# Performance work log

Hardware: AMD Instinct MI355X
Metric: run time of the kernel (lower is better)

The kernel has to match this reference:

```python
import jax, jax.numpy as jnp
import numpy as np

B, T, C, H = 4, 2048, 1024, 16
HD = C // H  # head_dim = 64


def setup_inputs() -> dict:
    key = jax.random.key(0)
    k1, k2, k3, k4, k5 = jax.random.split(key, 5)
    s = 1.0 / np.sqrt(C)
    return {
        "x": jax.random.normal(k1, (B, T, C), dtype=jnp.float32),
        "Wqkv": jax.random.normal(k2, (C, 3 * C), dtype=jnp.float32) * s,
        "bqkv": jnp.zeros((3 * C,), dtype=jnp.float32),
        "Wproj": jax.random.normal(k3, (C, C), dtype=jnp.float32) * s,
        "bproj": jnp.zeros((C,), dtype=jnp.float32),
    }


def reference(x, Wqkv, bqkv, Wproj, bproj):
    b, t, c = x.shape
    qkv = x @ Wqkv + bqkv                      # [B,T,3C]
    q, k, v = jnp.split(qkv, 3, axis=-1)
    # [B,T,C] -> [B,H,T,HD]
    q = q.reshape(b, t, H, HD).transpose(0, 2, 1, 3)
    k = k.reshape(b, t, H, HD).transpose(0, 2, 1, 3)
    v = v.reshape(b, t, H, HD).transpose(0, 2, 1, 3)
    att = jnp.einsum("bhqd,bhkd->bhqk", q, k) * (1.0 / np.sqrt(HD))
    causal = jnp.tril(jnp.ones((t, t), dtype=bool))
    att = jnp.where(causal[None, None], att, -jnp.inf)
    att = jax.nn.softmax(att, axis=-1)
    # dropout p=0.0 (eval) -> identity
    y = jnp.einsum("bhqk,bhkd->bhqd", att, v)  # [B,H,T,HD]
    y = y.transpose(0, 2, 1, 3).reshape(b, t, c)
    return y @ Wproj + bproj
```

## Files before the change

### kernel.cpp

```cpp
#include <hip/hip_runtime.h>


typedef unsigned short u16;
typedef short short8_t __attribute__((ext_vector_type(8)));
typedef float f32x4 __attribute__((ext_vector_type(4)));
typedef float f32x16 __attribute__((ext_vector_type(16)));
typedef unsigned int u32x4 __attribute__((ext_vector_type(4)));

#define B_ 4
#define T_ 2048
#define C_ 1024
#define H_ 16
#define HD_ 64
#define QSCALE 0.18033688011112042f

__device__ __forceinline__ u16 f32_to_bf16(float f) {
  unsigned int u = __float_as_uint(f);
  u += 0x7fffu + ((u >> 16) & 1u);
  return (u16)(u >> 16);
}

__device__ __forceinline__ void async_copy16(const void* g, void* l) {
  __builtin_amdgcn_global_load_lds((const __attribute__((address_space(1))) void*)g,
                                   (__attribute__((address_space(3))) void*)l, 16, 0, 0);
}

__device__ __forceinline__ void wave_barrier() { asm volatile("s_barrier" ::: "memory"); }
template <int N>
__device__ __forceinline__ void wait_vmcnt() {
  asm volatile("s_waitcnt vmcnt(%0)" ::"i"(N) : "memory");
}

__device__ __forceinline__ unsigned int cvt_pk_bf16(float lo, float hi) {
  unsigned int r;
  asm("v_cvt_pk_bf16_f32 %0, %1, %2" : "=v"(r) : "v"(lo), "v"(hi));
  return r;
}

__device__ __forceinline__ void transpose_tile(const float* __restrict__ in,
                                               u16* __restrict__ out, int K, int N, int bx, int by,
                                               float (*tile)[33], int tid) {
  int nb = bx * 32, kb = by * 32;
  int c = tid & 31, r0 = tid >> 5;
#pragma unroll
  for (int rr = 0; rr < 4; ++rr) {
    int r = r0 + rr * 8;
    tile[r][c] = in[(size_t)(kb + r) * N + nb + c];
  }
  __syncthreads();
#pragma unroll
  for (int rr = 0; rr < 4; ++rr) {
    int r = r0 + rr * 8;
    out[(size_t)(nb + r) * K + kb + c] = f32_to_bf16(tile[c][r]);
  }
}

__global__ void prep_kernel(const float* __restrict__ x, u16* __restrict__ Xb,
                            const float* __restrict__ Wqkv, u16* __restrict__ WqkvT,
                            const float* __restrict__ Wproj, u16* __restrict__ WprojT) {
  __shared__ float tile[32][33];
  int id = blockIdx.x;
  int tid = threadIdx.x;
  if (id < 8192) {
    int i = id * 256 + tid;
    float4 v = ((const float4*)x)[i];
    unsigned int a = (unsigned int)f32_to_bf16(v.x) | ((unsigned int)f32_to_bf16(v.y) << 16);
    unsigned int b = (unsigned int)f32_to_bf16(v.z) | ((unsigned int)f32_to_bf16(v.w) << 16);
    ((uint2*)Xb)[i] = make_uint2(a, b);
  } else if (id < 11264) {
    int t = id - 8192;
    transpose_tile(Wqkv, WqkvT, C_, 3 * C_, t % 96, t / 96, tile, tid);
  } else {
    int t = id - 11264;
    transpose_tile(Wproj, WprojT, C_, C_, t % 32, t / 32, tile, tid);
  }
}

__device__ __forceinline__ void stage_tile(const u16* __restrict__ A, const u16* __restrict__ Bt,
                                           int K, int m0, int n0, int k0, char* buf, int tid) {
#pragma unroll
  for (int it = 0; it < 2; ++it) {
    int j = it * 256 + tid;
    int row = j >> 2;
    int ch = ((j & 3) ^ (row >> 1)) & 3;
    async_copy16(A + (size_t)(m0 + row) * K + k0 + ch * 8, buf + j * 16);
    async_copy16(Bt + (size_t)(n0 + row) * K + k0 + ch * 8, buf + 8192 + j * 16);
  }
}

__device__ __forceinline__ void gemm_mainloop(const u16* __restrict__ A, const u16* __restrict__ Bt,
                                              int K, int m0, int n0, char* smem,
                                              f32x4 (&acc)[4][4]) {
  int tid = threadIdx.x;
  int lane = tid & 63, wave = tid >> 6;
  int quad = lane >> 4, l15 = lane & 15;
  int waveM = wave >> 1, waveN = wave & 1;
  int nIter = K >> 5;
  stage_tile(A, Bt, K, m0, n0, 0, smem, tid);
  stage_tile(A, Bt, K, m0, n0, 32, smem + 16384, tid);
  int cur = 0;
  for (int ki = 0; ki < nIter; ++ki) {
    int nxt2 = cur + 2;
    if (nxt2 >= 3) nxt2 -= 3;
    if (ki + 2 < nIter) {
      stage_tile(A, Bt, K, m0, n0, (ki + 2) << 5, smem + nxt2 * 16384, tid);
      wait_vmcnt<8>();
    } else if (ki + 2 == nIter) {
      wait_vmcnt<4>();
    } else {
      wait_vmcnt<0>();
    }
    wave_barrier();
    char* bufc = smem + cur * 16384;
    short8_t af[4], bfr[4];
#pragma unroll
    for (int mt = 0; mt < 4; ++mt) {
      int row = waveM * 64 + mt * 16 + l15;
      af[mt] = *(const short8_t*)(bufc + row * 64 + (((quad ^ (row >> 1)) & 3) << 4));
    }
#pragma unroll
    for (int nt = 0; nt < 4; ++nt) {
      int row = waveN * 64 + nt * 16 + l15;
      bfr[nt] = *(const short8_t*)(bufc + 8192 + row * 64 + (((quad ^ (row >> 1)) & 3) << 4));
    }
    __builtin_amdgcn_s_setprio(1);
#pragma unroll
    for (int mt = 0; mt < 4; ++mt)
#pragma unroll
      for (int nt = 0; nt < 4; ++nt)
        acc[mt][nt] = __builtin_amdgcn_mfma_f32_16x16x32_bf16(af[mt], bfr[nt], acc[mt][nt], 0, 0, 0);
    __builtin_amdgcn_s_setprio(0);
    wave_barrier();
    cur = cur + 1;
    if (cur == 3) cur = 0;
  }
}

__global__ __launch_bounds__(256, 3) void gemm1_kernel(const u16* __restrict__ A,
                                                       const u16* __restrict__ Bt,
                                                       const float* __restrict__ bias,
                                                       u16* __restrict__ Qo, u16* __restrict__ Ko,
                                                       u16* __restrict__ Vo) {
  __shared__ __align__(128) char smem[49152];
  f32x4 acc[4][4];
#pragma unroll
  for (int mt = 0; mt < 4; ++mt)
#pragma unroll
    for (int nt = 0; nt < 4; ++nt) acc[mt][nt] = (f32x4){0.f, 0.f, 0.f, 0.f};
  int m0 = blockIdx.y * 128, n0 = blockIdx.x * 128;
  gemm_mainloop(A, Bt, C_, m0, n0, smem, acc);

  int lane = threadIdx.x & 63, wave = threadIdx.x >> 6;
  int quad = lane >> 4, l15 = lane & 15;
  int waveM = wave >> 1, waveN = wave & 1;

  if (n0 < 2048) {
#pragma unroll
    for (int nt = 0; nt < 4; ++nt) {
      int n = n0 + waveN * 64 + nt * 16;
      int which = n >> 10;
      int rem = n & 1023;
      int head = rem >> 6;
      int d = (rem & 63) + l15;
      float bv = bias[n + l15];
      float sc = (which == 0) ? QSCALE : 1.0f;
      u16* dst = (which == 0) ? Qo : Ko;
#pragma unroll
      for (int mt = 0; mt < 4; ++mt) {
#pragma unroll
        for (int r = 0; r < 4; ++r) {
          int token = m0 + waveM * 64 + mt * 16 + quad * 4 + r;
          int b = token >> 11, t = token & 2047;
          dst[(((size_t)(b * H_ + head)) * T_ + t) * HD_ + d] =
              f32_to_bf16((acc[mt][nt][r] + bv) * sc);
        }
      }
    }
  } else {
    __syncthreads();
    char* W = smem + wave * 8192;
#pragma unroll
    for (int nt = 0; nt < 4; ++nt) {
      int nl = nt * 16 + l15;
      float bv = bias[n0 + waveN * 64 + nl];
#pragma unroll
      for (int mt = 0; mt < 4; ++mt) {
        int g = mt * 4 + quad;
        int pc = ((g >> 1) ^ (nl & 7)) & 7;
        uint2 pv;
        pv.x = (unsigned int)f32_to_bf16(acc[mt][nt][0] + bv) |
               ((unsigned int)f32_to_bf16(acc[mt][nt][1] + bv) << 16);
        pv.y = (unsigned int)f32_to_bf16(acc[mt][nt][2] + bv) |
               ((unsigned int)f32_to_bf16(acc[mt][nt][3] + bv) << 16);
        *(uint2*)(W + nl * 128 + pc * 16 + (g & 1) * 8) = pv;
      }
    }
    int b = m0 >> 11;
#pragma unroll
    for (int i = 0; i < 8; ++i) {
      int jj = i * 64 + lane;
      int nl = jj >> 3;
      int c = jj & 7;
      int pc = c ^ (nl & 7);
      uint4 v = *(const uint4*)(W + nl * 128 + pc * 16);
      int rem = (n0 - 2048) + waveN * 64 + nl;
      int head = rem >> 6, dd = rem & 63;
      int t0 = (m0 & 2047) + waveM * 64 + c * 8;
      *(uint4*)(Vo + ((size_t)(b * H_ + head) * HD_ + dd) * T_ + t0) = v;
    }
  }
}

__global__ __launch_bounds__(256, 3) void gemm2_kernel(const u16* __restrict__ A,
                                                       const u16* __restrict__ Bt,
                                                       const float* __restrict__ bias,
                                                       float* __restrict__ out) {
  __shared__ __align__(128) char smem[49152];
  f32x4 acc[4][4];
#pragma unroll
  for (int mt = 0; mt < 4; ++mt)
#pragma unroll
    for (int nt = 0; nt < 4; ++nt) acc[mt][nt] = (f32x4){0.f, 0.f, 0.f, 0.f};
  int m0 = blockIdx.y * 128, n0 = blockIdx.x * 128;
  gemm_mainloop(A, Bt, C_, m0, n0, smem, acc);

  int lane = threadIdx.x & 63, wave = threadIdx.x >> 6;
  int quad = lane >> 4, l15 = lane & 15;
  int waveM = wave >> 1, waveN = wave & 1;
#pragma unroll
  for (int nt = 0; nt < 4; ++nt) {
    int col = n0 + waveN * 64 + nt * 16 + l15;
    float bv = bias[col];
#pragma unroll
    for (int mt = 0; mt < 4; ++mt) {
#pragma unroll
      for (int r = 0; r < 4; ++r) {
        int token = m0 + waveM * 64 + mt * 16 + quad * 4 + r;
        out[(size_t)token * C_ + col] = acc[mt][nt][r] + bv;
      }
    }
  }
}

__device__ __forceinline__ void stage_kv(const u16* __restrict__ Kb, const u16* __restrict__ Vb,
                                         int kt, char* Ksb, char* Vsb, int tid) {
#pragma unroll
  for (int it = 0; it < 2; ++it) {
    int j = it * 256 + tid;
    int row = j >> 3;
    int ch = (j & 7) ^ (row & 7);
    async_copy16(Kb + (size_t)(kt * 64 + row) * HD_ + ch * 8, Ksb + j * 16);
    async_copy16(Vb + (size_t)row * T_ + kt * 64 + ch * 8, Vsb + j * 16);
  }
}

__device__ __forceinline__ float softmax_block(f32x16& s, int kbase_g, bool diag, int qrow_g,
                                               int hi) {
  float lsum = 0.f;
#pragma unroll
  for (int r = 0; r < 16; ++r) {
    float p = __builtin_amdgcn_exp2f(s[r]);
    if (diag) {
      int kpos = kbase_g + (r & 3) + 8 * (r >> 2) + 4 * hi;
      if (kpos > qrow_g) p = 0.f;
    }
    s[r] = p;
    lsum += p;
  }
  return lsum;
}

__device__ __forceinline__ void pack_pfrags(const f32x16& s, int hi, short8_t& f0, short8_t& f1) {
  unsigned int pk[8], qk[8];
#pragma unroll
  for (int j = 0; j < 8; ++j) pk[j] = cvt_pk_bf16(s[2 * j], s[2 * j + 1]);
#pragma unroll
  for (int j = 0; j < 8; ++j) qk[j] = (unsigned int)__shfl_xor((int)pk[j], 32);
  u32x4 w0, w1;
  if (hi == 0) {
    w0 = (u32x4){pk[0], pk[1], qk[0], qk[1]};
    w1 = (u32x4){pk[4], pk[5], qk[4], qk[5]};
  } else {
    w0 = (u32x4){qk[2], qk[3], pk[2], pk[3]};
    w1 = (u32x4){qk[6], qk[7], pk[6], pk[7]};
  }
  f0 = __builtin_bit_cast(short8_t, w0);
  f1 = __builtin_bit_cast(short8_t, w1);
}

#define MFMA32(a, b, c) __builtin_amdgcn_mfma_f32_32x32x16_bf16(a, b, c, 0, 0, 0)

__global__ __launch_bounds__(256, 3) void attn_kernel(const u16* __restrict__ Qg,
                                                      const u16* __restrict__ Kg,
                                                      const u16* __restrict__ Vg,
                                                      u16* __restrict__ Yg) {
  __shared__ __align__(128) char smem[32768];
  int tid = threadIdx.x;
  int wave = tid >> 6, lane = tid & 63;
  int l31 = lane & 31, hi = lane >> 5;
  int bh = blockIdx.x;
  int qt = 15 - blockIdx.y;
  int b = bh >> 4, h = bh & 15;
  const u16* Kb = Kg + (size_t)bh * T_ * HD_;
  const u16* Vb = Vg + (size_t)bh * HD_ * T_;
  int qrow = qt * 128 + wave * 32 + l31;

  short8_t qf[4];
#pragma unroll
  for (int f = 0; f < 4; ++f)
    qf[f] = *(const short8_t*)(Qg + ((size_t)bh * T_ + qrow) * HD_ + f * 16 + hi * 8);

  stage_kv(Kb, Vb, 0, smem, smem + 16384, tid);

  float l_lane = 0.f;
  f32x16 o0, o1;
#pragma unroll
  for (int i = 0; i < 16; ++i) {
    o0[i] = 0.f;
    o1[i] = 0.f;
  }

  int ktmax_blk = 2 * qt + 1;
  int ktmax_wave = 2 * qt + (wave >> 1);
  for (int kt = 0; kt <= ktmax_blk; ++kt) {
    int cur = kt & 1;
    char* Ksc = smem + cur * 8192;
    char* Vtc = smem + 16384 + cur * 8192;
    __syncthreads();
    if (kt < ktmax_blk)
      stage_kv(Kb, Vb, kt + 1, smem + (cur ^ 1) * 8192, smem + 16384 + (cur ^ 1) * 8192, tid);
    if (kt > ktmax_wave) continue;

    f32x16 s0, s1;
#pragma unroll
    for (int i = 0; i < 16; ++i) {
      s0[i] = 0.f;
      s1[i] = 0.f;
    }
    int swz7 = l31 & 7;
#pragma unroll
    for (int f = 0; f < 4; ++f) {
      int pc = (((f * 2 + hi) ^ swz7) & 7) << 4;
      short8_t kf0 = *(const short8_t*)(Ksc + l31 * 128 + pc);
      short8_t kf1 = *(const short8_t*)(Ksc + (32 + l31) * 128 + pc);
      s0 = MFMA32(kf0, qf[f], s0);
      s1 = MFMA32(kf1, qf[f], s1);
    }

    bool diag = (kt == ktmax_wave);
    l_lane += softmax_block(s0, kt * 64, diag, qrow, hi);
    l_lane += softmax_block(s1, kt * 64 + 32, diag, qrow, hi);

    short8_t pf0, pf1, pf2, pf3;
    pack_pfrags(s0, hi, pf0, pf1);
    pack_pfrags(s1, hi, pf2, pf3);

#pragma unroll
    for (int f = 0; f < 4; ++f) {
      int pc = (((f * 2 + hi) ^ swz7) & 7) << 4;
      short8_t va = *(const short8_t*)(Vtc + l31 * 128 + pc);
      short8_t vb = *(const short8_t*)(Vtc + (32 + l31) * 128 + pc);
      short8_t pf = (f == 0) ? pf0 : (f == 1) ? pf1 : (f == 2) ? pf2 : pf3;
      o0 = MFMA32(pf, va, o0);
      o1 = MFMA32(pf, vb, o1);
    }
  }

  float lc = l_lane + __shfl_xor(l_lane, 32);
#pragma unroll
  for (int r = 0; r < 16; ++r) {
    int q_r = (r & 3) + 8 * (r >> 2) + 4 * hi;
    float inv = 1.0f / __shfl(lc, q_r);
    int t = qt * 128 + wave * 32 + q_r;
    size_t base = ((size_t)(b * T_ + t)) * C_ + h * HD_;
    Yg[base + l31] = f32_to_bf16(o0[r] * inv);
    Yg[base + 32 + l31] = f32_to_bf16(o1[r] * inv);
  }
}

extern "C" void kernel_launch(void* const* d_in, const int* in_sizes, int n_in,
                              void* d_out, int out_size, void* d_ws, size_t ws_size,
                              hipStream_t stream) {
  (void)in_sizes; (void)n_in; (void)out_size; (void)ws_size;
  const float* x = (const float*)d_in[0];
  const float* Wqkv = (const float*)d_in[1];
  const float* bqkv = (const float*)d_in[2];
  const float* Wproj = (const float*)d_in[3];
  const float* bproj = (const float*)d_in[4];
  float* out = (float*)d_out;
  char* ws = (char*)d_ws;

  u16* Xb = (u16*)ws;
  u16* WqkvT = (u16*)(ws + 16777216);
  u16* WprojT = (u16*)(ws + 16777216 + 6291456);
  u16* Q = (u16*)(ws + 25165824);
  u16* K = Q + 8388608;
  u16* V = K + 8388608;
  u16* Y = Xb;

  prep_kernel<<<12288, 256, 0, stream>>>(x, Xb, Wqkv, WqkvT, Wproj, WprojT);
  gemm1_kernel<<<dim3(24, 64), 256, 0, stream>>>(Xb, WqkvT, bqkv, Q, K, V);
  attn_kernel<<<dim3(64, 16), 256, 0, stream>>>(Q, K, V, Y);
  gemm2_kernel<<<dim3(8, 64), 256, 0, stream>>>(Y, WprojT, bproj, out);
}
```

Measured before the change: 243.4 us.

## Process two 32-row query tiles per wave to reuse K/V fragments

Each wave now handles 64 query rows (two 32-row sub-tiles) instead of 32, so a block covers 256 queries and the grid halves along the query axis. Each K and V fragment read from shared memory feeds twice as many MFMAs, which cuts LDS traffic and K/V staging per query. In exchange, register pressure roughly doubles, so launch bounds drop to 2 blocks per CU. The coarser causal tiles also mean more idle waves near the diagonal and fewer blocks to balance the load.

```diff
diff --git a/kernel.cpp b/kernel.cpp
--- a/kernel.cpp
+++ b/kernel.cpp
@@ -290,7 +290,7 @@
 
 #define MFMA32(a, b, c) __builtin_amdgcn_mfma_f32_32x32x16_bf16(a, b, c, 0, 0, 0)
 
-__global__ __launch_bounds__(256, 3) void attn_kernel(const u16* __restrict__ Qg,
+__global__ __launch_bounds__(256, 2) void attn_kernel(const u16* __restrict__ Qg,
                                                       const u16* __restrict__ Kg,
                                                       const u16* __restrict__ Vg,
                                                       u16* __restrict__ Yg) {
@@ -299,29 +299,34 @@
   int wave = tid >> 6, lane = tid & 63;
   int l31 = lane & 31, hi = lane >> 5;
   int bh = blockIdx.x;
-  int qt = 15 - blockIdx.y;
+  int qt = 7 - blockIdx.y;
   int b = bh >> 4, h = bh & 15;
   const u16* Kb = Kg + (size_t)bh * T_ * HD_;
   const u16* Vb = Vg + (size_t)bh * HD_ * T_;
-  int qrow = qt * 128 + wave * 32 + l31;
-
-  short8_t qf[4];
-#pragma unroll
-  for (int f = 0; f < 4; ++f)
-    qf[f] = *(const short8_t*)(Qg + ((size_t)bh * T_ + qrow) * HD_ + f * 16 + hi * 8);
+  int qrowA = qt * 256 + wave * 64 + l31;
+  int qrowB = qrowA + 32;
+
+  short8_t qfA[4], qfB[4];
+#pragma unroll
+  for (int f = 0; f < 4; ++f) {
+    qfA[f] = *(const short8_t*)(Qg + ((size_t)bh * T_ + qrowA) * HD_ + f * 16 + hi * 8);
+    qfB[f] = *(const short8_t*)(Qg + ((size_t)bh * T_ + qrowB) * HD_ + f * 16 + hi * 8);
+  }
 
   stage_kv(Kb, Vb, 0, smem, smem + 16384, tid);
 
-  float l_lane = 0.f;
-  f32x16 o0, o1;
+  float lA = 0.f, lB = 0.f;
+  f32x16 oA0, oA1, oB0, oB1;
 #pragma unroll
   for (int i = 0; i < 16; ++i) {
-    o0[i] = 0.f;
-    o1[i] = 0.f;
-  }
-
-  int ktmax_blk = 2 * qt + 1;
-  int ktmax_wave = 2 * qt + (wave >> 1);
+    oA0[i] = 0.f;
+    oA1[i] = 0.f;
+    oB0[i] = 0.f;
+    oB1[i] = 0.f;
+  }
+
+  int ktmax_blk = 4 * qt + 3;
+  int ktmax_wave = 4 * qt + wave;
   for (int kt = 0; kt <= ktmax_blk; ++kt) {
     int cur = kt & 1;
     char* Ksc = smem + cur * 8192;
@@ -331,11 +336,13 @@
       stage_kv(Kb, Vb, kt + 1, smem + (cur ^ 1) * 8192, smem + 16384 + (cur ^ 1) * 8192, tid);
     if (kt > ktmax_wave) continue;
 
-    f32x16 s0, s1;
+    f32x16 sA0, sA1, sB0, sB1;
 #pragma unroll
     for (int i = 0; i < 16; ++i) {
-      s0[i] = 0.f;
-      s1[i] = 0.f;
+      sA0[i] = 0.f;
+      sA1[i] = 0.f;
+      sB0[i] = 0.f;
+      sB1[i] = 0.f;
     }
     int swz7 = l31 & 7;
 #pragma unroll
@@ -343,38 +350,50 @@
       int pc = (((f * 2 + hi) ^ swz7) & 7) << 4;
       short8_t kf0 = *(const short8_t*)(Ksc + l31 * 128 + pc);
       short8_t kf1 = *(const short8_t*)(Ksc + (32 + l31) * 128 + pc);
-      s0 = MFMA32(kf0, qf[f], s0);
-      s1 = MFMA32(kf1, qf[f], s1);
+      sA0 = MFMA32(kf0, qfA[f], sA0);
+      sA1 = MFMA32(kf1, qfA[f], sA1);
+      sB0 = MFMA32(kf0, qfB[f], sB0);
+      sB1 = MFMA32(kf1, qfB[f], sB1);
     }
 
     bool diag = (kt == ktmax_wave);
-    l_lane += softmax_block(s0, kt * 64, diag, qrow, hi);
-    l_lane += softmax_block(s1, kt * 64 + 32, diag, qrow, hi);
-
-    short8_t pf0, pf1, pf2, pf3;
-    pack_pfrags(s0, hi, pf0, pf1);
-    pack_pfrags(s1, hi, pf2, pf3);
+    lA += softmax_block(sA0, kt * 64, diag, qrowA, hi);
+    lA += softmax_block(sA1, kt * 64 + 32, diag, qrowA, hi);
+    short8_t pfA[4];
+    pack_pfrags(sA0, hi, pfA[0], pfA[1]);
+    pack_pfrags(sA1, hi, pfA[2], pfA[3]);
+    lB += softmax_block(sB0, kt * 64, diag, qrowB, hi);
+    lB += softmax_block(sB1, kt * 64 + 32, diag, qrowB, hi);
+    short8_t pfB[4];
+    pack_pfrags(sB0, hi, pfB[0], pfB[1]);
+    pack_pfrags(sB1, hi, pfB[2], pfB[3]);
 
 #pragma unroll
     for (int f = 0; f < 4; ++f) {
       int pc = (((f * 2 + hi) ^ swz7) & 7) << 4;
       short8_t va = *(const short8_t*)(Vtc + l31 * 128 + pc);
       short8_t vb = *(const short8_t*)(Vtc + (32 + l31) * 128 + pc);
-      short8_t pf = (f == 0) ? pf0 : (f == 1) ? pf1 : (f == 2) ? pf2 : pf3;
-      o0 = MFMA32(pf, va, o0);
-      o1 = MFMA32(pf, vb, o1);
-    }
-  }
-
-  float lc = l_lane + __shfl_xor(l_lane, 32);
+      oA0 = MFMA32(pfA[f], va, oA0);
+      oA1 = MFMA32(pfA[f], vb, oA1);
+      oB0 = MFMA32(pfB[f], va, oB0);
+      oB1 = MFMA32(pfB[f], vb, oB1);
+    }
+  }
+
+  float lcA = lA + __shfl_xor(lA, 32);
+  float lcB = lB + __shfl_xor(lB, 32);
 #pragma unroll
   for (int r = 0; r < 16; ++r) {
     int q_r = (r & 3) + 8 * (r >> 2) + 4 * hi;
-    float inv = 1.0f / __shfl(lc, q_r);
-    int t = qt * 128 + wave * 32 + q_r;
-    size_t base = ((size_t)(b * T_ + t)) * C_ + h * HD_;
-    Yg[base + l31] = f32_to_bf16(o0[r] * inv);
-    Yg[base + 32 + l31] = f32_to_bf16(o1[r] * inv);
+    float invA = 1.0f / __shfl(lcA, q_r);
+    float invB = 1.0f / __shfl(lcB, q_r);
+    int tA = qt * 256 + wave * 64 + q_r;
+    size_t baseA = ((size_t)(b * T_ + tA)) * C_ + h * HD_;
+    Yg[baseA + l31] = f32_to_bf16(oA0[r] * invA);
+    Yg[baseA + 32 + l31] = f32_to_bf16(oA1[r] * invA);
+    size_t baseB = baseA + (size_t)32 * C_;
+    Yg[baseB + l31] = f32_to_bf16(oB0[r] * invB);
+    Yg[baseB + 32 + l31] = f32_to_bf16(oB1[r] * invB);
   }
 }
 
@@ -400,6 +419,6 @@
 
   prep_kernel<<<12288, 256, 0, stream>>>(x, Xb, Wqkv, WqkvT, Wproj, WprojT);
   gemm1_kernel<<<dim3(24, 64), 256, 0, stream>>>(Xb, WqkvT, bqkv, Q, K, V);
-  attn_kernel<<<dim3(64, 16), 256, 0, stream>>>(Q, K, V, Y);
+  attn_kernel<<<dim3(64, 8), 256, 0, stream>>>(Q, K, V, Y);
   gemm2_kernel<<<dim3(8, 64), 256, 0, stream>>>(Y, WprojT, bproj, out);
 }
```

Measured after the change: 260.2 us. 6.9% more time.
